# Optimization experiments

Hardware: AMD Instinct MI355X
Metric: run time of the kernel (lower is better)

Reference implementation:

```python
import jax, jax.numpy as jnp
import numpy as np


def setup_inputs() -> dict:
    key = jax.random.key(0)
    k1, k2, k3 = jax.random.split(key, 3)
    Na, Nb, K, D = 1024, 1024, 256, 128
    a = jax.random.normal(k1, (Na, D), dtype=jnp.float32)
    b = jax.random.normal(k2, (Nb, D), dtype=jnp.float32)
    feats = jax.random.normal(k3, (K, D), dtype=jnp.float32)
    return {"a": a, "b": b, "feats": feats}


def reference(a, b, feats):
    # mode='ignorematch'
    a_fk = a @ feats.T            # [Na, K]
    b_fk = b @ feats.T            # [Nb, K]
    a_e = a_fk[:, None, :]        # [Na, 1, K]
    b_e = b_fk[None, :, :]        # [1, Nb, K]
    mask = ((a_e > 0) & (b_e <= 0)).astype(a_fk.dtype)  # [Na, Nb, K]
    result = jnp.sum(a_e * mask, axis=2)                # [Na, Nb]
    return result
```

## Files before the change

### kernel.cpp

```cpp
#include <hip/hip_runtime.h>
#include <hip/hip_bf16.h>

typedef __attribute__((ext_vector_type(4))) float f32x4;
typedef __attribute__((ext_vector_type(4))) double f64x4;
typedef __attribute__((ext_vector_type(8))) short short8;

#define NA 1024
#define NB 1024
#define KF 256
#define DIM 128

#define PRB 64
#define PCB 16
#define PP 132

__global__ __launch_bounds__(256) void proj_kernel(
    const float* __restrict__ a, const float* __restrict__ b,
    const float* __restrict__ feats,
    __hip_bfloat16* __restrict__ P, __hip_bfloat16* __restrict__ M)
{
    __shared__ float Xs[PRB][PP];
    __shared__ float Fs[PCB][PP];

    const int t = threadIdx.x;
    const int rowBlk = blockIdx.x >> 4;
    const int colBlk = blockIdx.x & 15;
    const int row0 = rowBlk * PRB;
    const int col0 = colBlk * PCB;

    const bool isA = row0 < NA;
    const float* __restrict__ src = isA ? a : b;
    const int r0 = isA ? row0 : row0 - NA;

#pragma unroll
    for (int i = 0; i < 8; ++i) {
        int idx = t + i * 256;
        int r = idx >> 5, c4 = idx & 31;
        *(f32x4*)&Xs[r][c4 * 4] =
            *(const f32x4*)(src + (size_t)(r0 + r) * DIM + c4 * 4);
    }
#pragma unroll
    for (int i = 0; i < 2; ++i) {
        int idx = t + i * 256;
        int r = idx >> 5, c4 = idx & 31;
        *(f32x4*)&Fs[r][c4 * 4] =
            *(const f32x4*)(feats + (size_t)(col0 + r) * DIM + c4 * 4);
    }
    __syncthreads();

    const int l = t & 63;
    const int w = t >> 6;
    const int fr = l & 15;
    const int fq = l >> 4;

    f64x4 probe = {0.0, 0.0, 0.0, 0.0};
    probe = __builtin_amdgcn_mfma_f64_16x16x4f64((double)fr, 1.0, probe, 0, 0, 0);
    probe = __builtin_amdgcn_mfma_f64_16x16x4f64(1.0, 64.0 * (double)fr, probe, 0, 0, 0);

    const float* __restrict__ xrow = &Xs[w * 16 + fr][fq];
    const float* __restrict__ frow = &Fs[fr][fq];

    f64x4 acc0 = {0.0, 0.0, 0.0, 0.0};
    f64x4 acc1 = {0.0, 0.0, 0.0, 0.0};

#pragma unroll
    for (int s = 0; s < 32; s += 2) {
        double a0 = (double)xrow[s * 4];
        double b0 = (double)frow[s * 4];
        acc0 = __builtin_amdgcn_mfma_f64_16x16x4f64(a0, b0, acc0, 0, 0, 0);
        double a1 = (double)xrow[s * 4 + 4];
        double b1 = (double)frow[s * 4 + 4];
        acc1 = __builtin_amdgcn_mfma_f64_16x16x4f64(a1, b1, acc1, 0, 0, 0);
    }

    if (isA) {
#pragma unroll
        for (int r = 0; r < 4; ++r) {
            int code = (int)probe[r];
            int m = (code >> 2) & 15;
            int n = code >> 8;
            double v = acc0[r] + acc1[r];
            float vr = (v > 0.0) ? (float)v : 0.0f;
            P[(size_t)(r0 + w * 16 + m) * KF + col0 + n] = __float2bfloat16(vr);
        }
    } else {
#pragma unroll
        for (int r = 0; r < 4; ++r) {
            int code = (int)probe[r];
            int m = (code >> 2) & 15;
            int n = code >> 8;
            double v = acc0[r] + acc1[r];
            float vr = (v <= 0.0) ? 1.0f : 0.0f;
            M[(size_t)(r0 + w * 16 + m) * KF + col0 + n] = __float2bfloat16(vr);
        }
    }
}

__global__ __launch_bounds__(256) void gemm_kernel(
    const __hip_bfloat16* __restrict__ P, const __hip_bfloat16* __restrict__ M,
    float* __restrict__ out)
{
    __shared__ short LA[64][264];
    __shared__ short LB[64][264];
    const int t = threadIdx.x;
    const int row0 = blockIdx.y * 64;
    const int col0 = blockIdx.x * 64;
    const short* Pa = (const short*)P;
    const short* Mb = (const short*)M;

#pragma unroll
    for (int i = 0; i < 8; ++i) {
        int c = t + i * 256;
        int row = c >> 5;
        int c8 = (c & 31) << 3;
        *(short8*)&LA[row][c8] = *(const short8*)(Pa + (size_t)(row0 + row) * KF + c8);
        *(short8*)&LB[row][c8] = *(const short8*)(Mb + (size_t)(col0 + row) * KF + c8);
    }
    __syncthreads();

    const int lane = t & 63;
    const int wid = t >> 6;
    const int wr = (wid >> 1) * 32;
    const int wc = (wid & 1) * 32;
    const int fr = lane & 15;
    const int fq = lane >> 4;

    f32x4 acc[2][2];
#pragma unroll
    for (int m = 0; m < 2; ++m)
#pragma unroll
        for (int n = 0; n < 2; ++n)
            acc[m][n] = (f32x4){0.f, 0.f, 0.f, 0.f};

#pragma unroll
    for (int kk = 0; kk < KF / 32; ++kk) {
        const int kb = kk * 32 + fq * 8;
        short8 a0 = *(const short8*)&LA[wr + fr][kb];
        short8 a1 = *(const short8*)&LA[wr + 16 + fr][kb];
        short8 b0 = *(const short8*)&LB[wc + fr][kb];
        short8 b1 = *(const short8*)&LB[wc + 16 + fr][kb];
        acc[0][0] = __builtin_amdgcn_mfma_f32_16x16x32_bf16(a0, b0, acc[0][0], 0, 0, 0);
        acc[0][1] = __builtin_amdgcn_mfma_f32_16x16x32_bf16(a0, b1, acc[0][1], 0, 0, 0);
        acc[1][0] = __builtin_amdgcn_mfma_f32_16x16x32_bf16(a1, b0, acc[1][0], 0, 0, 0);
        acc[1][1] = __builtin_amdgcn_mfma_f32_16x16x32_bf16(a1, b1, acc[1][1], 0, 0, 0);
    }

#pragma unroll
    for (int m = 0; m < 2; ++m)
#pragma unroll
        for (int n = 0; n < 2; ++n)
#pragma unroll
            for (int r = 0; r < 4; ++r) {
                int row = row0 + wr + m * 16 + fq * 4 + r;
                int col = col0 + wc + n * 16 + fr;
                out[(size_t)row * NB + col] = acc[m][n][r];
            }
}

extern "C" void kernel_launch(void* const* d_in, const int* in_sizes, int n_in,
                              void* d_out, int out_size, void* d_ws, size_t ws_size,
                              hipStream_t stream) {
    const float* a = (const float*)d_in[0];
    const float* b = (const float*)d_in[1];
    const float* feats = (const float*)d_in[2];
    float* out = (float*)d_out;
    __hip_bfloat16* P = (__hip_bfloat16*)d_ws;
    __hip_bfloat16* M = P + (size_t)NA * KF;

    proj_kernel<<<dim3(512), dim3(256), 0, stream>>>(a, b, feats, P, M);
    gemm_kernel<<<dim3(NB / 64, NA / 64), dim3(256), 0, stream>>>(P, M, out);
}
```

Before: 14.31 us.

## Fuse projection and GEMM into one persistent kernel with a global barrier

Merges the projection kernel and the bf16 GEMM kernel into a single 256-block launch. An atomic-counter grid barrier separates the two phases, and shared memory is reused through a union. The projection tiling becomes 32x64 per block, so each wave computes a 16x32 tile with f64 MFMA. This removes the second kernel launch and the gap between kernels, but adds a memset, a spin barrier, and reliance on all 256 blocks being resident at once.

```diff
diff --git a/kernel.cpp b/kernel.cpp
--- a/kernel.cpp
+++ b/kernel.cpp
@@ -9,152 +9,159 @@
 #define NB 1024
 #define KF 256
 #define DIM 128
+#define GRID 256
 
-#define PRB 64
-#define PCB 16
-#define PP 132
 
-__global__ __launch_bounds__(256) void proj_kernel(
+union SharedU {
+    struct { float Xs[32][132]; float Fs[64][132]; } pa;
+    struct { short LA[64][264]; short LB[64][264]; } pb;
+};
+
+__global__ __launch_bounds__(256) void fused_kernel(
     const float* __restrict__ a, const float* __restrict__ b,
     const float* __restrict__ feats,
-    __hip_bfloat16* __restrict__ P, __hip_bfloat16* __restrict__ M)
+    __hip_bfloat16* __restrict__ P, __hip_bfloat16* __restrict__ M,
+    unsigned int* __restrict__ cnt,
+    float* __restrict__ out)
 {
-    __shared__ float Xs[PRB][PP];
-    __shared__ float Fs[PCB][PP];
+    __shared__ SharedU sh;
+    const int t = threadIdx.x;
+    const int bb = blockIdx.x;
 
-    const int t = threadIdx.x;
-    const int rowBlk = blockIdx.x >> 4;
-    const int colBlk = blockIdx.x & 15;
-    const int row0 = rowBlk * PRB;
-    const int col0 = colBlk * PCB;
-
-    const bool isA = row0 < NA;
-    const float* __restrict__ src = isA ? a : b;
-    const int r0 = isA ? row0 : row0 - NA;
+    {
+        const int rb = bb >> 2;
+        const int cb = bb & 3;
+        const int row0 = rb * 32;
+        const int col0 = cb * 64;
+        const bool isA = row0 < NA;
+        const float* __restrict__ src = isA ? a : b;
+        const int r0 = isA ? row0 : row0 - NA;
 
 #pragma unroll
-    for (int i = 0; i < 8; ++i) {
-        int idx = t + i * 256;
-        int r = idx >> 5, c4 = idx & 31;
-        *(f32x4*)&Xs[r][c4 * 4] =
-            *(const f32x4*)(src + (size_t)(r0 + r) * DIM + c4 * 4);
+        for (int i = 0; i < 4; ++i) {
+            int idx = t + i * 256;
+            int r = idx >> 5, c4 = idx & 31;
+            *(f32x4*)&sh.pa.Xs[r][c4 * 4] =
+                *(const f32x4*)(src + (size_t)(r0 + r) * DIM + c4 * 4);
+        }
+#pragma unroll
+        for (int i = 0; i < 8; ++i) {
+            int idx = t + i * 256;
+            int r = idx >> 5, c4 = idx & 31;
+            *(f32x4*)&sh.pa.Fs[r][c4 * 4] =
+                *(const f32x4*)(feats + (size_t)(col0 + r) * DIM + c4 * 4);
+        }
+        __syncthreads();
+
+        const int l = t & 63, w = t >> 6;
+        const int fr = l & 15, fq = l >> 4;
+
+        f64x4 probe = {0.0, 0.0, 0.0, 0.0};
+        probe = __builtin_amdgcn_mfma_f64_16x16x4f64((double)fr, 1.0, probe, 0, 0, 0);
+        probe = __builtin_amdgcn_mfma_f64_16x16x4f64(1.0, 64.0 * (double)fr, probe, 0, 0, 0);
+
+        const int wrow = (w & 1) * 16;
+        const int wcol = (w >> 1) * 32;
+        const float* __restrict__ xr  = &sh.pa.Xs[wrow + fr][fq];
+        const float* __restrict__ fp0 = &sh.pa.Fs[wcol + fr][fq];
+        const float* __restrict__ fp1 = &sh.pa.Fs[wcol + 16 + fr][fq];
+
+        f64x4 acc[2][2] = {{{0.,0.,0.,0.},{0.,0.,0.,0.}},{{0.,0.,0.,0.},{0.,0.,0.,0.}}};
+#pragma unroll
+        for (int s = 0; s < 32; s += 2) {
+            double x0 = (double)xr[s * 4],     x1 = (double)xr[s * 4 + 4];
+            double f00 = (double)fp0[s * 4],   f01 = (double)fp0[s * 4 + 4];
+            double f10 = (double)fp1[s * 4],   f11 = (double)fp1[s * 4 + 4];
+            acc[0][0] = __builtin_amdgcn_mfma_f64_16x16x4f64(x0, f00, acc[0][0], 0, 0, 0);
+            acc[1][0] = __builtin_amdgcn_mfma_f64_16x16x4f64(x0, f10, acc[1][0], 0, 0, 0);
+            acc[0][1] = __builtin_amdgcn_mfma_f64_16x16x4f64(x1, f01, acc[0][1], 0, 0, 0);
+            acc[1][1] = __builtin_amdgcn_mfma_f64_16x16x4f64(x1, f11, acc[1][1], 0, 0, 0);
+        }
+
+#pragma unroll
+        for (int tt = 0; tt < 2; ++tt) {
+#pragma unroll
+            for (int r = 0; r < 4; ++r) {
+                int code = (int)probe[r];
+                int m = (code >> 2) & 15;
+                int n = code >> 8;
+                double v = acc[tt][0][r] + acc[tt][1][r];
+                size_t off = (size_t)(r0 + wrow + m) * KF + col0 + wcol + tt * 16 + n;
+                if (isA) {
+                    float vr = (v > 0.0) ? (float)v : 0.0f;
+                    P[off] = __float2bfloat16(vr);
+                } else {
+                    float vr = (v <= 0.0) ? 1.0f : 0.0f;
+                    M[off] = __float2bfloat16(vr);
+                }
+            }
+        }
     }
-#pragma unroll
-    for (int i = 0; i < 2; ++i) {
-        int idx = t + i * 256;
-        int r = idx >> 5, c4 = idx & 31;
-        *(f32x4*)&Fs[r][c4 * 4] =
-            *(const f32x4*)(feats + (size_t)(col0 + r) * DIM + c4 * 4);
+
+    __threadfence();
+    __syncthreads();
+    if (t == 0) {
+        __hip_atomic_fetch_add(cnt, 1u, __ATOMIC_ACQ_REL, __HIP_MEMORY_SCOPE_AGENT);
+        while (__hip_atomic_load(cnt, __ATOMIC_ACQUIRE, __HIP_MEMORY_SCOPE_AGENT) < GRID) {
+            __builtin_amdgcn_s_sleep(1);
+        }
     }
     __syncthreads();
 
-    const int l = t & 63;
-    const int w = t >> 6;
-    const int fr = l & 15;
-    const int fq = l >> 4;
-
-    f64x4 probe = {0.0, 0.0, 0.0, 0.0};
-    probe = __builtin_amdgcn_mfma_f64_16x16x4f64((double)fr, 1.0, probe, 0, 0, 0);
-    probe = __builtin_amdgcn_mfma_f64_16x16x4f64(1.0, 64.0 * (double)fr, probe, 0, 0, 0);
-
-    const float* __restrict__ xrow = &Xs[w * 16 + fr][fq];
-    const float* __restrict__ frow = &Fs[fr][fq];
-
-    f64x4 acc0 = {0.0, 0.0, 0.0, 0.0};
-    f64x4 acc1 = {0.0, 0.0, 0.0, 0.0};
+    {
+        const int row0 = (bb >> 4) * 64;
+        const int col0 = (bb & 15) * 64;
+        const short* Pa = (const short*)P;
+        const short* Mb = (const short*)M;
 
 #pragma unroll
-    for (int s = 0; s < 32; s += 2) {
-        double a0 = (double)xrow[s * 4];
-        double b0 = (double)frow[s * 4];
-        acc0 = __builtin_amdgcn_mfma_f64_16x16x4f64(a0, b0, acc0, 0, 0, 0);
-        double a1 = (double)xrow[s * 4 + 4];
-        double b1 = (double)frow[s * 4 + 4];
-        acc1 = __builtin_amdgcn_mfma_f64_16x16x4f64(a1, b1, acc1, 0, 0, 0);
-    }
+        for (int i = 0; i < 8; ++i) {
+            int c = t + i * 256;
+            int row = c >> 5;
+            int c8 = (c & 31) << 3;
+            *(short8*)&sh.pb.LA[row][c8] = *(const short8*)(Pa + (size_t)(row0 + row) * KF + c8);
+            *(short8*)&sh.pb.LB[row][c8] = *(const short8*)(Mb + (size_t)(col0 + row) * KF + c8);
+        }
+        __syncthreads();
 
-    if (isA) {
+        const int lane = t & 63;
+        const int wid = t >> 6;
+        const int wr = (wid >> 1) * 32;
+        const int wc = (wid & 1) * 32;
+        const int fr = lane & 15;
+        const int fq = lane >> 4;
+
+        f32x4 acc[2][2];
 #pragma unroll
-        for (int r = 0; r < 4; ++r) {
-            int code = (int)probe[r];
-            int m = (code >> 2) & 15;
-            int n = code >> 8;
-            double v = acc0[r] + acc1[r];
-            float vr = (v > 0.0) ? (float)v : 0.0f;
-            P[(size_t)(r0 + w * 16 + m) * KF + col0 + n] = __float2bfloat16(vr);
-        }
-    } else {
+        for (int m = 0; m < 2; ++m)
 #pragma unroll
-        for (int r = 0; r < 4; ++r) {
-            int code = (int)probe[r];
-            int m = (code >> 2) & 15;
-            int n = code >> 8;
-            double v = acc0[r] + acc1[r];
-            float vr = (v <= 0.0) ? 1.0f : 0.0f;
-            M[(size_t)(r0 + w * 16 + m) * KF + col0 + n] = __float2bfloat16(vr);
-        }
-    }
-}
-
-__global__ __launch_bounds__(256) void gemm_kernel(
-    const __hip_bfloat16* __restrict__ P, const __hip_bfloat16* __restrict__ M,
-    float* __restrict__ out)
-{
-    __shared__ short LA[64][264];
-    __shared__ short LB[64][264];
-    const int t = threadIdx.x;
-    const int row0 = blockIdx.y * 64;
-    const int col0 = blockIdx.x * 64;
-    const short* Pa = (const short*)P;
-    const short* Mb = (const short*)M;
+            for (int n = 0; n < 2; ++n)
+                acc[m][n] = (f32x4){0.f, 0.f, 0.f, 0.f};
 
 #pragma unroll
-    for (int i = 0; i < 8; ++i) {
-        int c = t + i * 256;
-        int row = c >> 5;
-        int c8 = (c & 31) << 3;
-        *(short8*)&LA[row][c8] = *(const short8*)(Pa + (size_t)(row0 + row) * KF + c8);
-        *(short8*)&LB[row][c8] = *(const short8*)(Mb + (size_t)(col0 + row) * KF + c8);
-    }
-    __syncthreads();
-
-    const int lane = t & 63;
-    const int wid = t >> 6;
-    const int wr = (wid >> 1) * 32;
-    const int wc = (wid & 1) * 32;
-    const int fr = lane & 15;
-    const int fq = lane >> 4;
-
-    f32x4 acc[2][2];
-#pragma unroll
-    for (int m = 0; m < 2; ++m)
-#pragma unroll
-        for (int n = 0; n < 2; ++n)
-            acc[m][n] = (f32x4){0.f, 0.f, 0.f, 0.f};
+        for (int kk = 0; kk < KF / 32; ++kk) {
+            const int kb = kk * 32 + fq * 8;
+            short8 a0 = *(const short8*)&sh.pb.LA[wr + fr][kb];
+            short8 a1 = *(const short8*)&sh.pb.LA[wr + 16 + fr][kb];
+            short8 b0 = *(const short8*)&sh.pb.LB[wc + fr][kb];
+            short8 b1 = *(const short8*)&sh.pb.LB[wc + 16 + fr][kb];
+            acc[0][0] = __builtin_amdgcn_mfma_f32_16x16x32_bf16(a0, b0, acc[0][0], 0, 0, 0);
+            acc[0][1] = __builtin_amdgcn_mfma_f32_16x16x32_bf16(a0, b1, acc[0][1], 0, 0, 0);
+            acc[1][0] = __builtin_amdgcn_mfma_f32_16x16x32_bf16(a1, b0, acc[1][0], 0, 0, 0);
+            acc[1][1] = __builtin_amdgcn_mfma_f32_16x16x32_bf16(a1, b1, acc[1][1], 0, 0, 0);
+        }
 
 #pragma unroll
-    for (int kk = 0; kk < KF / 32; ++kk) {
-        const int kb = kk * 32 + fq * 8;
-        short8 a0 = *(const short8*)&LA[wr + fr][kb];
-        short8 a1 = *(const short8*)&LA[wr + 16 + fr][kb];
-        short8 b0 = *(const short8*)&LB[wc + fr][kb];
-        short8 b1 = *(const short8*)&LB[wc + 16 + fr][kb];
-        acc[0][0] = __builtin_amdgcn_mfma_f32_16x16x32_bf16(a0, b0, acc[0][0], 0, 0, 0);
-        acc[0][1] = __builtin_amdgcn_mfma_f32_16x16x32_bf16(a0, b1, acc[0][1], 0, 0, 0);
-        acc[1][0] = __builtin_amdgcn_mfma_f32_16x16x32_bf16(a1, b0, acc[1][0], 0, 0, 0);
-        acc[1][1] = __builtin_amdgcn_mfma_f32_16x16x32_bf16(a1, b1, acc[1][1], 0, 0, 0);
+        for (int m = 0; m < 2; ++m)
+#pragma unroll
+            for (int n = 0; n < 2; ++n)
+#pragma unroll
+                for (int r = 0; r < 4; ++r) {
+                    int row = row0 + wr + m * 16 + fq * 4 + r;
+                    int col = col0 + wc + n * 16 + fr;
+                    out[(size_t)row * NB + col] = acc[m][n][r];
+                }
     }
-
-#pragma unroll
-    for (int m = 0; m < 2; ++m)
-#pragma unroll
-        for (int n = 0; n < 2; ++n)
-#pragma unroll
-            for (int r = 0; r < 4; ++r) {
-                int row = row0 + wr + m * 16 + fq * 4 + r;
-                int col = col0 + wc + n * 16 + fr;
-                out[(size_t)row * NB + col] = acc[m][n][r];
-            }
 }
 
 extern "C" void kernel_launch(void* const* d_in, const int* in_sizes, int n_in,
@@ -166,7 +173,8 @@
     float* out = (float*)d_out;
     __hip_bfloat16* P = (__hip_bfloat16*)d_ws;
     __hip_bfloat16* M = P + (size_t)NA * KF;
+    unsigned int* cnt = (unsigned int*)((char*)d_ws + (1u << 20));
 
-    proj_kernel<<<dim3(512), dim3(256), 0, stream>>>(a, b, feats, P, M);
-    gemm_kernel<<<dim3(NB / 64, NA / 64), dim3(256), 0, stream>>>(P, M, out);
+    hipMemsetAsync(cnt, 0, sizeof(unsigned int), stream);
+    fused_kernel<<<dim3(GRID), dim3(256), 0, stream>>>(a, b, feats, P, M, cnt, out);
 }
```

Result: slower. 49.21 us (+244.0%).
